# Kernel tuning notes

Hardware: AMD Instinct MI355X
Metric: run time of the kernel (lower is better)

Reference implementation:

```python
import jax, jax.numpy as jnp
import numpy as np

NUM_HEADS = 16
HEAD_DIM = 256  # hidden_size // num_heads = 4096 // 16
SEQ = 240       # hardcoded in the original forward's view(1, 240, -1)
IN_SIZE = 4096
HID = 4096


def setup_inputs() -> dict:
    key = jax.random.key(0)
    ks = jax.random.split(key, 10)
    s = 0.02
    return {
        "input1": jax.random.normal(ks[0], (SEQ, IN_SIZE), jnp.float32),
        "input2": jax.random.normal(ks[1], (SEQ, IN_SIZE), jnp.float32),
        "Wq": jax.random.normal(ks[2], (HID, IN_SIZE), jnp.float32) * s,
        "bq": jax.random.normal(ks[3], (HID,), jnp.float32) * s,
        "Wk": jax.random.normal(ks[4], (HID, IN_SIZE), jnp.float32) * s,
        "bk": jax.random.normal(ks[5], (HID,), jnp.float32) * s,
        "Wv": jax.random.normal(ks[6], (HID, IN_SIZE), jnp.float32) * s,
        "bv": jax.random.normal(ks[7], (HID,), jnp.float32) * s,
    }


def reference(input1, input2, Wq, bq, Wk, bk, Wv, bv):
    # QKV projections (torch Linear: x @ W^T + b)
    q = input1 @ Wq.T + bq  # [S, HID]
    k = input2 @ Wk.T + bk
    v = input2 @ Wv.T + bv
    # [1, H, S, hd]
    q = q.reshape(1, SEQ, NUM_HEADS, HEAD_DIM).transpose(0, 2, 1, 3)
    k = k.reshape(1, SEQ, NUM_HEADS, HEAD_DIM).transpose(0, 2, 1, 3)
    v = v.reshape(1, SEQ, NUM_HEADS, HEAD_DIM).transpose(0, 2, 1, 3)
    scores = jnp.einsum("bhqd,bhkd->bhqk", q, k) / jnp.sqrt(jnp.float32(HEAD_DIM))
    w = jax.nn.softmax(scores, axis=-1)  # [1, H, Sq, Sk]
    # NOTE: the original does attention_weights.transpose(-2,-1) @ value, i.e. attn^T @ V
    out = jnp.einsum("bhqk,bhqd->bhkd", w, v)  # [1, H, Sk, hd]
    out = out.transpose(0, 2, 1, 3).reshape(1, SEQ, HID)
    # linear_out exists in __init__ but is never applied in forward.
    return out
```

## Files before the change

### kernel.cpp

```cpp
#include <hip/hip_runtime.h>
#include <hip/hip_bf16.h>

#define SEQ 240
#define HID 4096
#define NH 16
#define HD 256

typedef float f32x4 __attribute__((ext_vector_type(4)));
typedef short s16x8 __attribute__((ext_vector_type(8)));
typedef short s16x4 __attribute__((ext_vector_type(4)));

__device__ __forceinline__ short f2bf(float f) {
    unsigned u = __builtin_bit_cast(unsigned, f);
    unsigned r = u + 0x7FFFu + ((u >> 16) & 1u);
    return (short)(r >> 16);
}

__device__ __forceinline__ s16x8 cvt8(float4 a, float4 b) {
    s16x8 r;
    r[0] = f2bf(a.x); r[1] = f2bf(a.y); r[2] = f2bf(a.z); r[3] = f2bf(a.w);
    r[4] = f2bf(b.x); r[5] = f2bf(b.y); r[6] = f2bf(b.z); r[7] = f2bf(b.w);
    return r;
}

__global__ __launch_bounds__(256) void cvt_kernel(
    const float* __restrict__ in1, const float* __restrict__ in2,
    short* __restrict__ A1, short* __restrict__ A2)
{
    const int i = blockIdx.x * 256 + threadIdx.x;
    const float* __restrict__ src = blockIdx.y ? in2 : in1;
    short* __restrict__ dst = blockIdx.y ? A2 : A1;
    const int r = i >> 9;
    const int c = (i & 511) * 8;
    s16x8 v = (s16x8){0,0,0,0,0,0,0,0};
    if (r < SEQ) {
        float4 a = *(const float4*)&src[(size_t)r * HID + c];
        float4 b = *(const float4*)&src[(size_t)r * HID + c + 4];
        v = cvt8(a, b);
    }
    *(s16x8*)&dst[(size_t)r * HID + c] = v;
}

__global__ __launch_bounds__(256) void qkv_gemm(
    const short* __restrict__ A1, const short* __restrict__ A2,
    const float* __restrict__ Wq, const float* __restrict__ Wk,
    const float* __restrict__ Wv,
    float* __restrict__ pqk, float* __restrict__ pvt, int KC)
{
    const int g  = blockIdx.y;
    const int z  = blockIdx.z;
    const int nb = blockIdx.x * 64;
    const short* __restrict__ A = (g == 0) ? A1 : A2;
    const float* __restrict__ W = (g == 0) ? Wq : (g == 1) ? Wk : Wv;

    const int tid  = threadIdx.x;
    const int lane = tid & 63;
    const int wave = tid >> 6;
    const int wm   = wave >> 1;
    const int wn   = wave & 1;
    const int lr   = lane & 15;
    const int lg   = lane >> 4;

    __shared__ short As[2][256 * 64];
    __shared__ short Bs[2][64 * 64];

    f32x4 acc[8][2];
    #pragma unroll
    for (int m = 0; m < 8; ++m)
        #pragma unroll
        for (int n = 0; n < 2; ++n)
            acc[m][n] = (f32x4){0.f, 0.f, 0.f, 0.f};

    const int arow = tid >> 3;
    const int asl  = tid & 7;
    const int brow = tid >> 3;
    const int bsl  = tid & 7;

    s16x8 ra[8];
    float4 rb0[2], rb1[2];

    const int kbase = z * KC;
    const int NIT = KC / 64;

    auto LOADT = [&](int k0) {
        #pragma unroll
        for (int p = 0; p < 8; ++p)
            ra[p] = *(const s16x8*)&A[(size_t)(arow + p * 32) * HID + k0 + asl * 8];
        #pragma unroll
        for (int q = 0; q < 2; ++q) {
            const float* src = &W[(size_t)(nb + brow + q * 32) * HID + k0 + bsl * 8];
            rb0[q] = *(const float4*)src;
            rb1[q] = *(const float4*)(src + 4);
        }
    };
    auto STORET = [&](int b) {
        #pragma unroll
        for (int p = 0; p < 8; ++p) {
            const int r = arow + p * 32;
            *(s16x8*)&As[b][r * 64 + ((asl * 8) ^ ((r & 7) << 3))] = ra[p];
        }
        #pragma unroll
        for (int q = 0; q < 2; ++q) {
            const int r = brow + q * 32;
            *(s16x8*)&Bs[b][r * 64 + ((bsl * 8) ^ ((r & 7) << 3))] = cvt8(rb0[q], rb1[q]);
        }
    };

    LOADT(kbase);
    STORET(0);
    __syncthreads();

    for (int it = 0; it < NIT; ++it) {
        if (it + 1 < NIT) LOADT(kbase + (it + 1) * 64);
        const int b = it & 1;
        #pragma unroll
        for (int ks = 0; ks < 2; ++ks) {
            const int colx = ks * 32 + lg * 8;
            s16x8 af[8], bf[2];
            #pragma unroll
            for (int m = 0; m < 8; ++m) {
                const int r = wm * 128 + m * 16 + lr;
                af[m] = *(const s16x8*)&As[b][r * 64 + (colx ^ ((r & 7) << 3))];
            }
            #pragma unroll
            for (int n = 0; n < 2; ++n) {
                const int r = wn * 32 + n * 16 + lr;
                bf[n] = *(const s16x8*)&Bs[b][r * 64 + (colx ^ ((r & 7) << 3))];
            }
            #pragma unroll
            for (int m = 0; m < 8; ++m)
                #pragma unroll
                for (int n = 0; n < 2; ++n)
                    acc[m][n] = __builtin_amdgcn_mfma_f32_16x16x32_bf16(af[m], bf[n], acc[m][n], 0, 0, 0);
        }
        __syncthreads();
        if (it + 1 < NIT) {
            STORET((it + 1) & 1);
            __syncthreads();
        }
    }

    if (g == 2) {
        float* pout = pvt + (size_t)z * HID * SEQ;
        #pragma unroll
        for (int m = 0; m < 8; ++m) {
            const int row0 = wm * 128 + m * 16 + lg * 4;
            if (row0 >= SEQ) continue;
            #pragma unroll
            for (int n = 0; n < 2; ++n) {
                const int col = nb + wn * 32 + n * 16 + lr;
                float4 o = make_float4(acc[m][n][0], acc[m][n][1], acc[m][n][2], acc[m][n][3]);
                *(float4*)&pout[(size_t)col * SEQ + row0] = o;
            }
        }
    } else {
        float* pout = pqk + (size_t)(z * 2 + g) * SEQ * HID;
        #pragma unroll
        for (int m = 0; m < 8; ++m) {
            const int row0 = wm * 128 + m * 16 + lg * 4;
            if (row0 >= SEQ) continue;
            #pragma unroll
            for (int n = 0; n < 2; ++n) {
                const int col = nb + wn * 32 + n * 16 + lr;
                #pragma unroll
                for (int r = 0; r < 4; ++r)
                    pout[(size_t)(row0 + r) * HID + col] = acc[m][n][r];
            }
        }
    }
}

__global__ __launch_bounds__(256) void reduce_qk(
    const float* __restrict__ pqk,
    const float* __restrict__ bq, const float* __restrict__ bk,
    short* __restrict__ qb, short* __restrict__ kb, int KS)
{
    const int g   = blockIdx.y;
    const int idx = blockIdx.x * 256 + threadIdx.x;
    f32x4 s = (f32x4){0.f, 0.f, 0.f, 0.f};
    for (int z = 0; z < KS; ++z)
        s += *(const f32x4*)&pqk[(size_t)(z * 2 + g) * SEQ * HID + (size_t)idx * 4];
    const int n = (idx * 4) & (HID - 1);
    const float* bias = g ? bk : bq;
    s += *(const f32x4*)&bias[n];
    short* ob = g ? kb : qb;
    s16x4 o = (s16x4){f2bf(s[0]), f2bf(s[1]), f2bf(s[2]), f2bf(s[3])};
    *(s16x4*)&ob[(size_t)idx * 4] = o;
}

__global__ __launch_bounds__(256) void reduce_v(
    const float* __restrict__ pvt, const float* __restrict__ bv,
    short* __restrict__ vtb, int KS)
{
    const int idx = blockIdx.x * 256 + threadIdx.x;
    f32x4 s = (f32x4){0.f, 0.f, 0.f, 0.f};
    for (int z = 0; z < KS; ++z)
        s += *(const f32x4*)&pvt[(size_t)z * HID * SEQ + (size_t)idx * 4];
    const int n = idx / 60;
    const float b = bv[n];
    s16x4 o = (s16x4){f2bf(s[0] + b), f2bf(s[1] + b), f2bf(s[2] + b), f2bf(s[3] + b)};
    *(s16x4*)&vtb[(size_t)idx * 4] = o;
}

__global__ __launch_bounds__(256) void scores_kernel(
    const short* __restrict__ qb, const short* __restrict__ kb,
    short* __restrict__ ptb)
{
    const int it   = blockIdx.x;
    const int h    = blockIdx.y;
    const int tid  = threadIdx.x;
    const int lane = tid & 63;
    const int w    = tid >> 6;
    const int lr   = lane & 15;
    const int lg   = lane >> 4;
    const int jt0  = w * 4;
    const int NJT  = (w < 3) ? 4 : 3;

    __shared__ float redmax[4][16];
    __shared__ float redsum[4][16];

    f32x4 acc[4];
    #pragma unroll
    for (int j = 0; j < 4; ++j) acc[j] = (f32x4){0.f, 0.f, 0.f, 0.f};

    const int ib = it * 16;
    const short* qrow = &qb[(size_t)(ib + lr) * HID + h * HD + lg * 8];

    for (int d0 = 0; d0 < HD; d0 += 32) {
        s16x8 afr = *(const s16x8*)&qrow[d0];
        #pragma unroll
        for (int j = 0; j < 4; ++j) {
            if (j < NJT) {
                s16x8 bfr = *(const s16x8*)&kb[(size_t)((jt0 + j) * 16 + lr) * HID + h * HD + d0 + lg * 8];
                acc[j] = __builtin_amdgcn_mfma_f32_16x16x32_bf16(afr, bfr, acc[j], 0, 0, 0);
            }
        }
    }

    const float sc = 0.0625f;
    #pragma unroll
    for (int j = 0; j < 4; ++j) acc[j] *= sc;

    #pragma unroll
    for (int r = 0; r < 4; ++r) {
        float mx = -1e30f;
        #pragma unroll
        for (int j = 0; j < 4; ++j) if (j < NJT) mx = fmaxf(mx, acc[j][r]);
        #pragma unroll
        for (int s = 1; s < 16; s <<= 1) mx = fmaxf(mx, __shfl_xor(mx, s, 64));
        if (lr == 0) redmax[w][lg * 4 + r] = mx;
    }
    __syncthreads();
    #pragma unroll
    for (int r = 0; r < 4; ++r) {
        const int i = lg * 4 + r;
        float mx = fmaxf(fmaxf(redmax[0][i], redmax[1][i]),
                         fmaxf(redmax[2][i], redmax[3][i]));
        float sum = 0.f;
        #pragma unroll
        for (int j = 0; j < 4; ++j) {
            if (j < NJT) {
                float e = expf(acc[j][r] - mx);
                acc[j][r] = e;
                sum += e;
            }
        }
        #pragma unroll
        for (int s = 1; s < 16; s <<= 1) sum += __shfl_xor(sum, s, 64);
        if (lr == 0) redsum[w][i] = sum;
    }
    __syncthreads();
    #pragma unroll
    for (int r = 0; r < 4; ++r) {
        const int i = lg * 4 + r;
        const float inv = 1.f / (redsum[0][i] + redsum[1][i] + redsum[2][i] + redsum[3][i]);
        #pragma unroll
        for (int j = 0; j < 4; ++j) if (j < NJT) acc[j][r] *= inv;
    }
    #pragma unroll
    for (int j = 0; j < 4; ++j) {
        if (j < NJT) {
            const int jj = (jt0 + j) * 16 + lr;
            s16x4 o = (s16x4){f2bf(acc[j][0]), f2bf(acc[j][1]), f2bf(acc[j][2]), f2bf(acc[j][3])};
            *(s16x4*)&ptb[(size_t)(h * SEQ + jj) * SEQ + ib + lg * 4] = o;
        }
    }
}

__global__ __launch_bounds__(256) void pv_kernel(
    const short* __restrict__ ptb, const short* __restrict__ vtb,
    float* __restrict__ out)
{
    const int dt   = blockIdx.x;
    const int h    = blockIdx.y;
    const int tid  = threadIdx.x;
    const int lane = tid & 63;
    const int w    = tid >> 6;
    const int lr   = lane & 15;
    const int lg   = lane >> 4;
    const int NJT  = (w < 3) ? 4 : 3;

    f32x4 acc[4];
    #pragma unroll
    for (int j = 0; j < 4; ++j) acc[j] = (f32x4){0.f, 0.f, 0.f, 0.f};

    const short* vrow = &vtb[(size_t)(h * HD + dt * 16 + lr) * SEQ + lg * 8];

    for (int i0 = 0; i0 < 256; i0 += 32) {
        const bool ok = (i0 + lg * 8) < SEQ;
        s16x8 bfr = (s16x8){0,0,0,0,0,0,0,0};
        if (ok) bfr = *(const s16x8*)&vrow[i0];
        #pragma unroll
        for (int j = 0; j < 4; ++j) {
            if (j < NJT) {
                const int jt = w + j * 4;
                s16x8 afr = (s16x8){0,0,0,0,0,0,0,0};
                if (ok) afr = *(const s16x8*)&ptb[(size_t)(h * SEQ + jt * 16 + lr) * SEQ + i0 + lg * 8];
                acc[j] = __builtin_amdgcn_mfma_f32_16x16x32_bf16(afr, bfr, acc[j], 0, 0, 0);
            }
        }
    }

    #pragma unroll
    for (int j = 0; j < 4; ++j) {
        if (j < NJT) {
            const int jt = w + j * 4;
            #pragma unroll
            for (int r = 0; r < 4; ++r)
                out[(size_t)(jt * 16 + lg * 4 + r) * HID + h * HD + dt * 16 + lr] = acc[j][r];
        }
    }
}

extern "C" void kernel_launch(void* const* d_in, const int* in_sizes, int n_in,
                              void* d_out, int out_size, void* d_ws, size_t ws_size,
                              hipStream_t stream) {
    const float* in1 = (const float*)d_in[0];
    const float* in2 = (const float*)d_in[1];
    const float* Wq  = (const float*)d_in[2];
    const float* bq  = (const float*)d_in[3];
    const float* Wk  = (const float*)d_in[4];
    const float* bk  = (const float*)d_in[5];
    const float* Wv  = (const float*)d_in[6];
    const float* bv  = (const float*)d_in[7];
    float* out = (float*)d_out;

    char* w = (char*)d_ws;
    short* A1  = (short*)w;  w += (size_t)256 * HID * 2;
    short* A2  = (short*)w;  w += (size_t)256 * HID * 2;
    short* qb  = (short*)w;  w += (size_t)SEQ * HID * 2;
    short* kb  = (short*)w;  w += (size_t)SEQ * HID * 2;
    short* vtb = (short*)w;  w += (size_t)HID * SEQ * 2;
    short* ptb = (short*)w;  w += (size_t)NH * SEQ * SEQ * 2;
    float* pqk = (float*)w;
    const size_t fixed  = (size_t)(w - (char*)d_ws);
    const size_t perKS  = ((size_t)2 * SEQ * HID + (size_t)HID * SEQ) * sizeof(float);

    int KS = 1;
    if (fixed + 4 * perKS <= ws_size)      KS = 4;
    else if (fixed + 2 * perKS <= ws_size) KS = 2;
    const int KC = HID / KS;
    float* pvt = pqk + (size_t)KS * 2 * SEQ * HID;

    cvt_kernel<<<dim3(512, 2), 256, 0, stream>>>(in1, in2, A1, A2);
    qkv_gemm<<<dim3(64, 3, KS), 256, 0, stream>>>(A1, A2, Wq, Wk, Wv, pqk, pvt, KC);
    reduce_qk<<<dim3(960, 2), 256, 0, stream>>>(pqk, bq, bk, qb, kb, KS);
    reduce_v<<<960, 256, 0, stream>>>(pvt, bv, vtb, KS);
    scores_kernel<<<dim3(15, 16), 256, 0, stream>>>(qb, kb, ptb);
    pv_kernel<<<dim3(16, 16), 256, 0, stream>>>(ptb, vtb, out);
}
```

Measured before the change: 95.66 us.

## Load MFMA fragments directly from global memory in QKV GEMM, dropping LDS staging

Removes the double-buffered shared-memory tiles and barriers from the QKV projection GEMM. Each wave now loads its A (bf16) and W (fp32, converted in registers) fragments straight from global memory into MFMA operands, and launch bounds now request 3 blocks per SIMD. This removes LDS traffic and syncs and allows higher occupancy. In exchange it loses data reuse across waves (each W and A row is fetched by multiple waves), uses less coalesced strided global loads, and has no explicit prefetch to hide latency.

```diff
diff --git a/kernel.cpp b/kernel.cpp
--- a/kernel.cpp
+++ b/kernel.cpp
@@ -41,7 +41,7 @@
     *(s16x8*)&dst[(size_t)r * HID + c] = v;
 }
 
-__global__ __launch_bounds__(256) void qkv_gemm(
+__global__ __launch_bounds__(256, 3) void qkv_gemm(
     const short* __restrict__ A1, const short* __restrict__ A2,
     const float* __restrict__ Wq, const float* __restrict__ Wk,
     const float* __restrict__ Wv,
@@ -61,9 +61,6 @@
     const int lr   = lane & 15;
     const int lg   = lane >> 4;
 
-    __shared__ short As[2][256 * 64];
-    __shared__ short Bs[2][64 * 64];
-
     f32x4 acc[8][2];
     #pragma unroll
     for (int m = 0; m < 8; ++m)
@@ -71,72 +68,36 @@
         for (int n = 0; n < 2; ++n)
             acc[m][n] = (f32x4){0.f, 0.f, 0.f, 0.f};
 
-    const int arow = tid >> 3;
-    const int asl  = tid & 7;
-    const int brow = tid >> 3;
-    const int bsl  = tid & 7;
-
-    s16x8 ra[8];
-    float4 rb0[2], rb1[2];
+    const short* __restrict__ ap = A + (size_t)(wm * 128 + lr) * HID + lg * 8;
+    const float* __restrict__ wp = W + (size_t)(nb + wn * 32 + lr) * HID + lg * 8;
 
     const int kbase = z * KC;
     const int NIT = KC / 64;
 
-    auto LOADT = [&](int k0) {
-        #pragma unroll
-        for (int p = 0; p < 8; ++p)
-            ra[p] = *(const s16x8*)&A[(size_t)(arow + p * 32) * HID + k0 + asl * 8];
-        #pragma unroll
-        for (int q = 0; q < 2; ++q) {
-            const float* src = &W[(size_t)(nb + brow + q * 32) * HID + k0 + bsl * 8];
-            rb0[q] = *(const float4*)src;
-            rb1[q] = *(const float4*)(src + 4);
-        }
-    };
-    auto STORET = [&](int b) {
-        #pragma unroll
-        for (int p = 0; p < 8; ++p) {
-            const int r = arow + p * 32;
-            *(s16x8*)&As[b][r * 64 + ((asl * 8) ^ ((r & 7) << 3))] = ra[p];
-        }
-        #pragma unroll
-        for (int q = 0; q < 2; ++q) {
-            const int r = brow + q * 32;
-            *(s16x8*)&Bs[b][r * 64 + ((bsl * 8) ^ ((r & 7) << 3))] = cvt8(rb0[q], rb1[q]);
-        }
-    };
-
-    LOADT(kbase);
-    STORET(0);
-    __syncthreads();
-
-    for (int it = 0; it < NIT; ++it) {
-        if (it + 1 < NIT) LOADT(kbase + (it + 1) * 64);
-        const int b = it & 1;
+    for (int t = 0; t < NIT; ++t) {
+        const int k0 = kbase + t * 64;
+        float4 b0[2][2], b1[2][2];
+        #pragma unroll
+        for (int n = 0; n < 2; ++n)
+            #pragma unroll
+            for (int ks = 0; ks < 2; ++ks) {
+                const float* s = wp + (size_t)n * 16 * HID + k0 + ks * 32;
+                b0[n][ks] = *(const float4*)s;
+                b1[n][ks] = *(const float4*)(s + 4);
+            }
         #pragma unroll
         for (int ks = 0; ks < 2; ++ks) {
-            const int colx = ks * 32 + lg * 8;
-            s16x8 af[8], bf[2];
-            #pragma unroll
-            for (int m = 0; m < 8; ++m) {
-                const int r = wm * 128 + m * 16 + lr;
-                af[m] = *(const s16x8*)&As[b][r * 64 + (colx ^ ((r & 7) << 3))];
-            }
+            s16x8 af[8];
+            #pragma unroll
+            for (int m = 0; m < 8; ++m)
+                af[m] = *(const s16x8*)(ap + (size_t)m * 16 * HID + k0 + ks * 32);
             #pragma unroll
             for (int n = 0; n < 2; ++n) {
-                const int r = wn * 32 + n * 16 + lr;
-                bf[n] = *(const s16x8*)&Bs[b][r * 64 + (colx ^ ((r & 7) << 3))];
-            }
-            #pragma unroll
-            for (int m = 0; m < 8; ++m)
+                const s16x8 bf = cvt8(b0[n][ks], b1[n][ks]);
                 #pragma unroll
-                for (int n = 0; n < 2; ++n)
-                    acc[m][n] = __builtin_amdgcn_mfma_f32_16x16x32_bf16(af[m], bf[n], acc[m][n], 0, 0, 0);
-        }
-        __syncthreads();
-        if (it + 1 < NIT) {
-            STORET((it + 1) & 1);
-            __syncthreads();
+                for (int m = 0; m < 8; ++m)
+                    acc[m][n] = __builtin_amdgcn_mfma_f32_16x16x32_bf16(af[m], bf, acc[m][n], 0, 0, 0);
+            }
         }
     }
 
```

After: 181.4 us. +89.6%, slower.

## Shrink QKV GEMM N-tile and load A fragments directly from global memory

Applied to the files above, without the earlier changes.

The QKV projection GEMM now uses a 32-column N tile, with each wave owning 64 rows of M. A fragments are read straight from global memory (L2-resident bf16 activations) instead of being staged through LDS, so only the converted weight tile goes through shared memory. This cuts LDS use and register pressure so more blocks fit per CU (launch bounds 4), and doubles the grid to 128 column blocks. In exchange, each block rereads A from global/L2 with less reuse, and the direct fragment loads are strided across rows.

```diff
diff --git a/kernel.cpp b/kernel.cpp
--- a/kernel.cpp
+++ b/kernel.cpp
@@ -41,7 +41,7 @@
     *(s16x8*)&dst[(size_t)r * HID + c] = v;
 }
 
-__global__ __launch_bounds__(256) void qkv_gemm(
+__global__ __launch_bounds__(256, 4) void qkv_gemm(
     const short* __restrict__ A1, const short* __restrict__ A2,
     const float* __restrict__ Wq, const float* __restrict__ Wk,
     const float* __restrict__ Wv,
@@ -49,61 +49,41 @@
 {
     const int g  = blockIdx.y;
     const int z  = blockIdx.z;
-    const int nb = blockIdx.x * 64;
+    const int nb = blockIdx.x * 32;
     const short* __restrict__ A = (g == 0) ? A1 : A2;
     const float* __restrict__ W = (g == 0) ? Wq : (g == 1) ? Wk : Wv;
 
     const int tid  = threadIdx.x;
     const int lane = tid & 63;
-    const int wave = tid >> 6;
-    const int wm   = wave >> 1;
-    const int wn   = wave & 1;
+    const int wm   = tid >> 6;
     const int lr   = lane & 15;
     const int lg   = lane >> 4;
 
-    __shared__ short As[2][256 * 64];
-    __shared__ short Bs[2][64 * 64];
-
-    f32x4 acc[8][2];
-    #pragma unroll
-    for (int m = 0; m < 8; ++m)
+    __shared__ short Bs[2][32 * 64];
+
+    f32x4 acc[4][2];
+    #pragma unroll
+    for (int m = 0; m < 4; ++m)
         #pragma unroll
         for (int n = 0; n < 2; ++n)
             acc[m][n] = (f32x4){0.f, 0.f, 0.f, 0.f};
 
-    const int arow = tid >> 3;
-    const int asl  = tid & 7;
     const int brow = tid >> 3;
     const int bsl  = tid & 7;
 
-    s16x8 ra[8];
-    float4 rb0[2], rb1[2];
+    float4 rb0, rb1;
+    const float* __restrict__ wsrc = &W[(size_t)(nb + brow) * HID + bsl * 8];
+    const short* __restrict__ ap   = A + (size_t)(wm * 64 + lr) * HID + lg * 8;
 
     const int kbase = z * KC;
     const int NIT = KC / 64;
 
     auto LOADT = [&](int k0) {
-        #pragma unroll
-        for (int p = 0; p < 8; ++p)
-            ra[p] = *(const s16x8*)&A[(size_t)(arow + p * 32) * HID + k0 + asl * 8];
-        #pragma unroll
-        for (int q = 0; q < 2; ++q) {
-            const float* src = &W[(size_t)(nb + brow + q * 32) * HID + k0 + bsl * 8];
-            rb0[q] = *(const float4*)src;
-            rb1[q] = *(const float4*)(src + 4);
-        }
+        rb0 = *(const float4*)(wsrc + k0);
+        rb1 = *(const float4*)(wsrc + k0 + 4);
     };
     auto STORET = [&](int b) {
-        #pragma unroll
-        for (int p = 0; p < 8; ++p) {
-            const int r = arow + p * 32;
-            *(s16x8*)&As[b][r * 64 + ((asl * 8) ^ ((r & 7) << 3))] = ra[p];
-        }
-        #pragma unroll
-        for (int q = 0; q < 2; ++q) {
-            const int r = brow + q * 32;
-            *(s16x8*)&Bs[b][r * 64 + ((bsl * 8) ^ ((r & 7) << 3))] = cvt8(rb0[q], rb1[q]);
-        }
+        *(s16x8*)&Bs[b][brow * 64 + ((bsl * 8) ^ ((brow & 7) << 3))] = cvt8(rb0, rb1);
     };
 
     LOADT(kbase);
@@ -113,22 +93,21 @@
     for (int it = 0; it < NIT; ++it) {
         if (it + 1 < NIT) LOADT(kbase + (it + 1) * 64);
         const int b = it & 1;
+        const int k0 = kbase + it * 64;
         #pragma unroll
         for (int ks = 0; ks < 2; ++ks) {
             const int colx = ks * 32 + lg * 8;
-            s16x8 af[8], bf[2];
-            #pragma unroll
-            for (int m = 0; m < 8; ++m) {
-                const int r = wm * 128 + m * 16 + lr;
-                af[m] = *(const s16x8*)&As[b][r * 64 + (colx ^ ((r & 7) << 3))];
-            }
+            s16x8 af[4], bf[2];
+            #pragma unroll
+            for (int m = 0; m < 4; ++m)
+                af[m] = *(const s16x8*)(ap + (size_t)m * 16 * HID + k0 + ks * 32);
             #pragma unroll
             for (int n = 0; n < 2; ++n) {
-                const int r = wn * 32 + n * 16 + lr;
+                const int r = n * 16 + lr;
                 bf[n] = *(const s16x8*)&Bs[b][r * 64 + (colx ^ ((r & 7) << 3))];
             }
             #pragma unroll
-            for (int m = 0; m < 8; ++m)
+            for (int m = 0; m < 4; ++m)
                 #pragma unroll
                 for (int n = 0; n < 2; ++n)
                     acc[m][n] = __builtin_amdgcn_mfma_f32_16x16x32_bf16(af[m], bf[n], acc[m][n], 0, 0, 0);
@@ -143,12 +122,12 @@
     if (g == 2) {
         float* pout = pvt + (size_t)z * HID * SEQ;
         #pragma unroll
-        for (int m = 0; m < 8; ++m) {
-            const int row0 = wm * 128 + m * 16 + lg * 4;
+        for (int m = 0; m < 4; ++m) {
+            const int row0 = wm * 64 + m * 16 + lg * 4;
             if (row0 >= SEQ) continue;
             #pragma unroll
             for (int n = 0; n < 2; ++n) {
-                const int col = nb + wn * 32 + n * 16 + lr;
+                const int col = nb + n * 16 + lr;
                 float4 o = make_float4(acc[m][n][0], acc[m][n][1], acc[m][n][2], acc[m][n][3]);
                 *(float4*)&pout[(size_t)col * SEQ + row0] = o;
             }
@@ -156,12 +135,12 @@
     } else {
         float* pout = pqk + (size_t)(z * 2 + g) * SEQ * HID;
         #pragma unroll
-        for (int m = 0; m < 8; ++m) {
-            const int row0 = wm * 128 + m * 16 + lg * 4;
+        for (int m = 0; m < 4; ++m) {
+            const int row0 = wm * 64 + m * 16 + lg * 4;
             if (row0 >= SEQ) continue;
             #pragma unroll
             for (int n = 0; n < 2; ++n) {
-                const int col = nb + wn * 32 + n * 16 + lr;
+                const int col = nb + n * 16 + lr;
                 #pragma unroll
                 for (int r = 0; r < 4; ++r)
                     pout[(size_t)(row0 + r) * HID + col] = acc[m][n][r];
@@ -363,7 +342,7 @@
     float* pvt = pqk + (size_t)KS * 2 * SEQ * HID;
 
     cvt_kernel<<<dim3(512, 2), 256, 0, stream>>>(in1, in2, A1, A2);
-    qkv_gemm<<<dim3(64, 3, KS), 256, 0, stream>>>(A1, A2, Wq, Wk, Wv, pqk, pvt, KC);
+    qkv_gemm<<<dim3(128, 3, KS), 256, 0, stream>>>(A1, A2, Wq, Wk, Wv, pqk, pvt, KC);
     reduce_qk<<<dim3(960, 2), 256, 0, stream>>>(pqk, bq, bk, qb, kb, KS);
     reduce_v<<<960, 256, 0, stream>>>(pvt, bv, vtb, KS);
     scores_kernel<<<dim3(15, 16), 256, 0, stream>>>(qb, kb, ptb);
```

After: 157.7 us. 1.65x slower.
